# Kernel tuning notes

Measured on AMD Instinct MI355X. Metric: run time of the kernel, lower is better.

The kernel has to match this reference:

```python
import jax, jax.numpy as jnp
import numpy as np


def setup_inputs() -> dict:
    key = jax.random.key(0)
    k1, k2 = jax.random.split(key)
    B, N, M = 4, 8192, 8192
    xyz1 = jax.random.normal(k1, (B, N, 3), dtype=jnp.float32)
    xyz2 = jax.random.normal(k2, (B, M, 3), dtype=jnp.float32)
    th = jnp.float32(0.1)
    return {"xyz1": xyz1, "xyz2": xyz2, "th": th}


def reference(xyz1, xyz2, th):
    # Pairwise squared distances (B, N, M) via the expanded form
    x2 = jnp.sum(xyz1 * xyz1, axis=-1)                    # (B, N)
    y2 = jnp.sum(xyz2 * xyz2, axis=-1)                    # (B, M)
    cross = jnp.einsum('bnd,bmd->bnm', xyz1, xyz2)        # (B, N, M)
    dist = x2[:, :, None] + y2[:, None, :] - 2.0 * cross  # (B, N, M)
    # torch: distances is (B, M, N); min over dim=1 -> per-x min (our axis=2),
    #        min over dim=2 -> per-y min (our axis=1).
    d1 = jnp.min(dist, axis=2)                            # (B, N)
    d2 = jnp.min(dist, axis=1)                            # (B, M)
    d1 = jnp.where(d1 <= th, jnp.float32(0.0), d1)
    d2 = jnp.where(d2 <= th, jnp.float32(0.0), d2)
    return jnp.mean(d1, axis=1) + jnp.mean(d2, axis=1)    # (B,)
```

## Files before the change

kernel.cpp:

```cpp
#include <hip/hip_runtime.h>
#include <math.h>

#define NBATCH 4
#define NPTS   8192
#define TPB    1024
#define QPB    256
#define QPT    4
#define NSLICE (TPB / 64)
#define SLICEPTS (NPTS / NSLICE)
#define TILES  (NPTS / QPB)
#define NBLK   (2 * NBATCH * TILES)

typedef float v2f __attribute__((ext_vector_type(2)));

__device__ __forceinline__ float min3f(float a, float b, float c) {
    return fminf(fminf(a, b), c);
}

__global__ __launch_bounds__(TPB, 4) void chamfer_main(
    const float* __restrict__ xyz1,
    const float* __restrict__ xyz2,
    const float* __restrict__ thp,
    double* __restrict__ partial)
{
    __shared__ float sx[NPTS], sy[NPTS], sz[NPTS], sw[NPTS];
    __shared__ float part[NSLICE][QPB];
    __shared__ double wsum[NSLICE];

    const int bid  = blockIdx.x;
    const int tile = bid & (TILES - 1);
    const int rest = bid / TILES;
    const int b    = rest & (NBATCH - 1);
    const int dir  = rest >> 2;

    const float* q = (dir == 0 ? xyz1 : xyz2) + (size_t)b * NPTS * 3;
    const float* r = (dir == 0 ? xyz2 : xyz1) + (size_t)b * NPTS * 3;

    for (int i = threadIdx.x; i < NPTS; i += TPB) {
        float x = r[3 * i + 0], y = r[3 * i + 1], z = r[3 * i + 2];
        sx[i] = -2.0f * x;
        sy[i] = -2.0f * y;
        sz[i] = -2.0f * z;
        sw[i] = x * x + y * y + z * z;
    }
    __syncthreads();

    const int lane = threadIdx.x & 63;
    const int w    = threadIdx.x >> 6;
    const int q0   = tile * QPB + lane * QPT;

    float qx[QPT], qy[QPT], qz[QPT], m[QPT];
    #pragma unroll
    for (int k = 0; k < QPT; ++k) {
        qx[k] = q[3 * (q0 + k) + 0];
        qy[k] = q[3 * (q0 + k) + 1];
        qz[k] = q[3 * (q0 + k) + 2];
        m[k]  = INFINITY;
    }

    const int base = w * SLICEPTS;
    #pragma unroll 1
    for (int j = 0; j < SLICEPTS; j += 8) {
        float4 X0 = *(const float4*)&sx[base + j];
        float4 X1 = *(const float4*)&sx[base + j + 4];
        float4 Y0 = *(const float4*)&sy[base + j];
        float4 Y1 = *(const float4*)&sy[base + j + 4];
        float4 Z0 = *(const float4*)&sz[base + j];
        float4 Z1 = *(const float4*)&sz[base + j + 4];
        float4 W0 = *(const float4*)&sw[base + j];
        float4 W1 = *(const float4*)&sw[base + j + 4];

        v2f xp[4] = { {X0.x, X0.y}, {X0.z, X0.w}, {X1.x, X1.y}, {X1.z, X1.w} };
        v2f yp[4] = { {Y0.x, Y0.y}, {Y0.z, Y0.w}, {Y1.x, Y1.y}, {Y1.z, Y1.w} };
        v2f zp[4] = { {Z0.x, Z0.y}, {Z0.z, Z0.w}, {Z1.x, Z1.y}, {Z1.z, Z1.w} };
        v2f wp[4] = { {W0.x, W0.y}, {W0.z, W0.w}, {W1.x, W1.y}, {W1.z, W1.w} };

        #pragma unroll
        for (int k = 0; k < QPT; ++k) {
            v2f qxv = { qx[k], qx[k] };
            v2f qyv = { qy[k], qy[k] };
            v2f qzv = { qz[k], qz[k] };
            #pragma unroll
            for (int g = 0; g < 4; ++g) {
                v2f d = __builtin_elementwise_fma(qxv, xp[g],
                        __builtin_elementwise_fma(qyv, yp[g],
                        __builtin_elementwise_fma(qzv, zp[g], wp[g])));
                m[k] = min3f(m[k], d.x, d.y);
            }
        }
    }

    #pragma unroll
    for (int k = 0; k < QPT; ++k)
        part[w][lane * QPT + k] = m[k];
    __syncthreads();

    double val = 0.0;
    if (threadIdx.x < QPB) {
        const int ql = threadIdx.x;
        float mv = part[0][ql];
        #pragma unroll
        for (int s = 1; s < NSLICE; ++s) mv = fminf(mv, part[s][ql]);
        const int qi = tile * QPB + ql;
        const float Qx = q[3 * qi + 0], Qy = q[3 * qi + 1], Qz = q[3 * qi + 2];
        const float dmin = (Qx * Qx + Qy * Qy + Qz * Qz) + mv;
        const float th = *thp;
        val = (dmin <= th) ? 0.0 : (double)dmin;
    }

    for (int off = 32; off > 0; off >>= 1)
        val += __shfl_down(val, off, 64);
    if (lane == 0) wsum[w] = val;
    __syncthreads();
    if (threadIdx.x == 0) {
        double s = 0.0;
        #pragma unroll
        for (int i = 0; i < NSLICE; ++i) s += wsum[i];
        partial[bid] = s;
    }
}

__global__ void chamfer_finalize(const double* __restrict__ partial,
                                 float* __restrict__ out)
{
    const int b = threadIdx.x;
    if (b < NBATCH) {
        double s = 0.0;
        for (int dir = 0; dir < 2; ++dir)
            for (int t = 0; t < TILES; ++t)
                s += partial[(dir * NBATCH + b) * TILES + t];
        out[b] = (float)(s / (double)NPTS);
    }
}

extern "C" void kernel_launch(void* const* d_in, const int* in_sizes, int n_in,
                              void* d_out, int out_size, void* d_ws, size_t ws_size,
                              hipStream_t stream) {
    const float* xyz1 = (const float*)d_in[0];
    const float* xyz2 = (const float*)d_in[1];
    const float* thp  = (const float*)d_in[2];
    float* out        = (float*)d_out;
    double* partial   = (double*)d_ws;

    chamfer_main<<<NBLK, TPB, 0, stream>>>(xyz1, xyz2, thp, partial);
    chamfer_finalize<<<1, 64, 0, stream>>>(partial, out);
}
```

Measured before the change: 48.16 us.

## Register-block 16 queries per thread and split reference points across blocks

Each thread now holds 16 query points instead of 4 in registers, so every shared-memory load of reference points is reused across more FMAs. The reference set is split into 4 chunks across blocks (256 blocks of 512 threads), so LDS use per block drops. Per-query partial minima go to workspace, and a new per-batch finalize kernel combines them, applies the threshold, and reduces. The loop is software-pipelined with two register buffers. The costs are higher register pressure from 16 queries, the extra workspace traffic, and a heavier finalize kernel.

```diff
diff --git a/kernel.cpp b/kernel.cpp
--- a/kernel.cpp
+++ b/kernel.cpp
@@ -3,41 +3,76 @@
 
 #define NBATCH 4
 #define NPTS   8192
-#define TPB    1024
-#define QPB    256
-#define QPT    4
-#define NSLICE (TPB / 64)
-#define SLICEPTS (NPTS / NSLICE)
-#define TILES  (NPTS / QPB)
-#define NBLK   (2 * NBATCH * TILES)
+#define TPB    512
+#define NWAVE  (TPB / 64)
+#define QPB    1024
+#define QPT    16
+#define QTILES (NPTS / QPB)
+#define PSPLIT 4
+#define PPB    (NPTS / PSPLIT)
+#define SLICE  (PPB / NWAVE)
+#define NBLK   (2 * NBATCH * QTILES * PSPLIT)
 
 typedef float v2f __attribute__((ext_vector_type(2)));
+typedef float v4f __attribute__((ext_vector_type(4)));
 
-__device__ __forceinline__ float min3f(float a, float b, float c) {
-    return fminf(fminf(a, b), c);
+struct PG {
+    v4f x0, x1, y0, y1, z0, z1, w0, w1;
+};
+
+__device__ __forceinline__ PG loadpg(const float* sx, const float* sy,
+                                     const float* sz, const float* sw, int i) {
+    PG g;
+    g.x0 = *(const v4f*)&sx[i]; g.x1 = *(const v4f*)&sx[i + 4];
+    g.y0 = *(const v4f*)&sy[i]; g.y1 = *(const v4f*)&sy[i + 4];
+    g.z0 = *(const v4f*)&sz[i]; g.z1 = *(const v4f*)&sz[i + 4];
+    g.w0 = *(const v4f*)&sw[i]; g.w1 = *(const v4f*)&sw[i + 4];
+    return g;
 }
 
-__global__ __launch_bounds__(TPB, 4) void chamfer_main(
+__device__ __forceinline__ void comp(const PG& g, const v2f* qxv,
+                                     const v2f* qyv, const v2f* qzv, float* m) {
+    v2f xp[4] = { g.x0.lo, g.x0.hi, g.x1.lo, g.x1.hi };
+    v2f yp[4] = { g.y0.lo, g.y0.hi, g.y1.lo, g.y1.hi };
+    v2f zp[4] = { g.z0.lo, g.z0.hi, g.z1.lo, g.z1.hi };
+    v2f wp[4] = { g.w0.lo, g.w0.hi, g.w1.lo, g.w1.hi };
+    #pragma unroll
+    for (int k = 0; k < QPT; ++k) {
+        #pragma unroll
+        for (int gg = 0; gg < 4; ++gg) {
+            v2f d = __builtin_elementwise_fma(qxv[k], xp[gg],
+                    __builtin_elementwise_fma(qyv[k], yp[gg],
+                    __builtin_elementwise_fma(qzv[k], zp[gg], wp[gg])));
+            m[k] = fminf(fminf(m[k], d.x), d.y);
+        }
+    }
+}
+
+__global__ __launch_bounds__(TPB, 2) void chamfer_main(
     const float* __restrict__ xyz1,
     const float* __restrict__ xyz2,
-    const float* __restrict__ thp,
-    double* __restrict__ partial)
+    float* __restrict__ ws_part)
 {
-    __shared__ float sx[NPTS], sy[NPTS], sz[NPTS], sw[NPTS];
-    __shared__ float part[NSLICE][QPB];
-    __shared__ double wsum[NSLICE];
+    __shared__ float sx[PPB] __attribute__((aligned(16)));
+    __shared__ float sy[PPB] __attribute__((aligned(16)));
+    __shared__ float sz[PPB] __attribute__((aligned(16)));
+    __shared__ float sw[PPB] __attribute__((aligned(16)));
+    __shared__ float part[NWAVE][QPB];
 
     const int bid  = blockIdx.x;
-    const int tile = bid & (TILES - 1);
-    const int rest = bid / TILES;
-    const int b    = rest & (NBATCH - 1);
-    const int dir  = rest >> 2;
+    const int ph   = bid & (PSPLIT - 1);
+    const int r1   = bid >> 2;
+    const int tile = r1 & (QTILES - 1);
+    const int r2   = r1 >> 3;
+    const int b    = r2 & (NBATCH - 1);
+    const int dir  = r2 >> 2;
 
-    const float* q = (dir == 0 ? xyz1 : xyz2) + (size_t)b * NPTS * 3;
-    const float* r = (dir == 0 ? xyz2 : xyz1) + (size_t)b * NPTS * 3;
+    const float* q  = (dir == 0 ? xyz1 : xyz2) + (size_t)b * NPTS * 3;
+    const float* rp = (dir == 0 ? xyz2 : xyz1) + (size_t)b * NPTS * 3
+                      + (size_t)ph * PPB * 3;
 
-    for (int i = threadIdx.x; i < NPTS; i += TPB) {
-        float x = r[3 * i + 0], y = r[3 * i + 1], z = r[3 * i + 2];
+    for (int i = threadIdx.x; i < PPB; i += TPB) {
+        float x = rp[3 * i + 0], y = rp[3 * i + 1], z = rp[3 * i + 2];
         sx[i] = -2.0f * x;
         sy[i] = -2.0f * y;
         sz[i] = -2.0f * z;
@@ -49,86 +84,77 @@
     const int w    = threadIdx.x >> 6;
     const int q0   = tile * QPB + lane * QPT;
 
-    float qx[QPT], qy[QPT], qz[QPT], m[QPT];
+    v2f qxv[QPT], qyv[QPT], qzv[QPT];
+    float m[QPT];
     #pragma unroll
     for (int k = 0; k < QPT; ++k) {
-        qx[k] = q[3 * (q0 + k) + 0];
-        qy[k] = q[3 * (q0 + k) + 1];
-        qz[k] = q[3 * (q0 + k) + 2];
-        m[k]  = INFINITY;
+        float Qx = q[3 * (q0 + k) + 0];
+        float Qy = q[3 * (q0 + k) + 1];
+        float Qz = q[3 * (q0 + k) + 2];
+        qxv[k] = (v2f){ Qx, Qx };
+        qyv[k] = (v2f){ Qy, Qy };
+        qzv[k] = (v2f){ Qz, Qz };
+        m[k]   = INFINITY;
     }
 
-    const int base = w * SLICEPTS;
+    const int base = w * SLICE;
+    PG A = loadpg(sx, sy, sz, sw, base + 0);
+    PG B = loadpg(sx, sy, sz, sw, base + 8);
     #pragma unroll 1
-    for (int j = 0; j < SLICEPTS; j += 8) {
-        float4 X0 = *(const float4*)&sx[base + j];
-        float4 X1 = *(const float4*)&sx[base + j + 4];
-        float4 Y0 = *(const float4*)&sy[base + j];
-        float4 Y1 = *(const float4*)&sy[base + j + 4];
-        float4 Z0 = *(const float4*)&sz[base + j];
-        float4 Z1 = *(const float4*)&sz[base + j + 4];
-        float4 W0 = *(const float4*)&sw[base + j];
-        float4 W1 = *(const float4*)&sw[base + j + 4];
-
-        v2f xp[4] = { {X0.x, X0.y}, {X0.z, X0.w}, {X1.x, X1.y}, {X1.z, X1.w} };
-        v2f yp[4] = { {Y0.x, Y0.y}, {Y0.z, Y0.w}, {Y1.x, Y1.y}, {Y1.z, Y1.w} };
-        v2f zp[4] = { {Z0.x, Z0.y}, {Z0.z, Z0.w}, {Z1.x, Z1.y}, {Z1.z, Z1.w} };
-        v2f wp[4] = { {W0.x, W0.y}, {W0.z, W0.w}, {W1.x, W1.y}, {W1.z, W1.w} };
-
-        #pragma unroll
-        for (int k = 0; k < QPT; ++k) {
-            v2f qxv = { qx[k], qx[k] };
-            v2f qyv = { qy[k], qy[k] };
-            v2f qzv = { qz[k], qz[k] };
-            #pragma unroll
-            for (int g = 0; g < 4; ++g) {
-                v2f d = __builtin_elementwise_fma(qxv, xp[g],
-                        __builtin_elementwise_fma(qyv, yp[g],
-                        __builtin_elementwise_fma(qzv, zp[g], wp[g])));
-                m[k] = min3f(m[k], d.x, d.y);
-            }
-        }
+    for (int j = 0; j < SLICE - 16; j += 16) {
+        comp(A, qxv, qyv, qzv, m);
+        A = loadpg(sx, sy, sz, sw, base + j + 16);
+        comp(B, qxv, qyv, qzv, m);
+        B = loadpg(sx, sy, sz, sw, base + j + 24);
     }
+    comp(A, qxv, qyv, qzv, m);
+    comp(B, qxv, qyv, qzv, m);
 
     #pragma unroll
     for (int k = 0; k < QPT; ++k)
         part[w][lane * QPT + k] = m[k];
     __syncthreads();
 
-    double val = 0.0;
-    if (threadIdx.x < QPB) {
-        const int ql = threadIdx.x;
+    for (int ql = threadIdx.x; ql < QPB; ql += TPB) {
         float mv = part[0][ql];
         #pragma unroll
-        for (int s = 1; s < NSLICE; ++s) mv = fminf(mv, part[s][ql]);
+        for (int s = 1; s < NWAVE; ++s) mv = fminf(mv, part[s][ql]);
         const int qi = tile * QPB + ql;
         const float Qx = q[3 * qi + 0], Qy = q[3 * qi + 1], Qz = q[3 * qi + 2];
-        const float dmin = (Qx * Qx + Qy * Qy + Qz * Qz) + mv;
-        const float th = *thp;
-        val = (dmin <= th) ? 0.0 : (double)dmin;
+        ws_part[(size_t)bid * QPB + ql] = (Qx * Qx + Qy * Qy + Qz * Qz) + mv;
     }
+}
 
+__global__ __launch_bounds__(QPB) void chamfer_finalize(
+    const float* __restrict__ ws_part,
+    const float* __restrict__ thp,
+    float* __restrict__ out)
+{
+    __shared__ double wsum[QPB / 64];
+    const int b = blockIdx.x;
+    const float th = *thp;
+    double acc = 0.0;
+    for (int dir = 0; dir < 2; ++dir) {
+        for (int t = 0; t < QTILES; ++t) {
+            const size_t gb = ((size_t)((dir * NBATCH + b) * QTILES + t)) * PSPLIT;
+            const int ql = threadIdx.x;
+            float mv =            ws_part[(gb + 0) * QPB + ql];
+            mv = fminf(mv, ws_part[(gb + 1) * QPB + ql]);
+            mv = fminf(mv, ws_part[(gb + 2) * QPB + ql]);
+            mv = fminf(mv, ws_part[(gb + 3) * QPB + ql]);
+            acc += (mv <= th) ? 0.0 : (double)mv;
+        }
+    }
     for (int off = 32; off > 0; off >>= 1)
-        val += __shfl_down(val, off, 64);
-    if (lane == 0) wsum[w] = val;
+        acc += __shfl_down(acc, off, 64);
+    const int lane = threadIdx.x & 63;
+    const int w    = threadIdx.x >> 6;
+    if (lane == 0) wsum[w] = acc;
     __syncthreads();
     if (threadIdx.x == 0) {
         double s = 0.0;
         #pragma unroll
-        for (int i = 0; i < NSLICE; ++i) s += wsum[i];
-        partial[bid] = s;
-    }
-}
-
-__global__ void chamfer_finalize(const double* __restrict__ partial,
-                                 float* __restrict__ out)
-{
-    const int b = threadIdx.x;
-    if (b < NBATCH) {
-        double s = 0.0;
-        for (int dir = 0; dir < 2; ++dir)
-            for (int t = 0; t < TILES; ++t)
-                s += partial[(dir * NBATCH + b) * TILES + t];
+        for (int i = 0; i < QPB / 64; ++i) s += wsum[i];
         out[b] = (float)(s / (double)NPTS);
     }
 }
@@ -140,8 +166,8 @@
     const float* xyz2 = (const float*)d_in[1];
     const float* thp  = (const float*)d_in[2];
     float* out        = (float*)d_out;
-    double* partial   = (double*)d_ws;
+    float* ws_part    = (float*)d_ws;
 
-    chamfer_main<<<NBLK, TPB, 0, stream>>>(xyz1, xyz2, thp, partial);
-    chamfer_finalize<<<1, 64, 0, stream>>>(partial, out);
+    chamfer_main<<<NBLK, TPB, 0, stream>>>(xyz1, xyz2, ws_part);
+    chamfer_finalize<<<NBATCH, QPB, 0, stream>>>(ws_part, thp, out);
 }
```

Result: slower. 62.77 us (+30.3%).
